# Kernel tuning notes

Hardware: AMD Instinct MI355X
Metric: run time of the kernel (lower is better)

## Reference

```python
import jax, jax.numpy as jnp
import numpy as np

B = 8192
G, K, D = 8, 1024, 64  # num_codebooks, codebook_size, code_dim
INIT_SCALE = 0.1


def setup_inputs() -> dict:
    key = jax.random.key(0)
    kz, kc = jax.random.split(key)
    z = jax.random.normal(kz, (B, G * D), dtype=jnp.float32)
    codebook = jax.random.uniform(kc, (G, K, D), dtype=jnp.float32,
                                  minval=-INIT_SCALE, maxval=INIT_SCALE)
    return {"z": z, "codebook": codebook}


def reference(z, codebook):
    # Eval-mode forward of GroupedVectorQuantizer (no EMA buffer mutation).
    b = z.shape[0]
    g, k, d = codebook.shape
    zg = z.reshape(b, g, d)                       # [B,G,D]
    # squared L2 distance via ||z||^2 + ||c||^2 - 2 z.c (avoids [B,G,K,D] diff tensor)
    z2 = jnp.sum(zg * zg, axis=-1, keepdims=True)           # [B,G,1]
    c2 = jnp.sum(codebook * codebook, axis=-1)[None]        # [1,G,K]
    zc = jnp.einsum('bgd,gkd->bgk', zg, codebook)           # [B,G,K]
    dist = z2 + c2 - 2.0 * zc                               # [B,G,K]
    indices = jnp.argmin(dist, axis=-1)                     # [B,G] int32
    # gather nearest codes per group
    zq = codebook[jnp.arange(g)[None, :], indices]          # [B,G,D]
    commitment_loss = jnp.mean((zg - jax.lax.stop_gradient(zq)) ** 2)
    codebook_loss = jnp.zeros((), dtype=z.dtype)
    # straight-through estimator
    z_st = zg + jax.lax.stop_gradient(zq - zg)
    quantized_flat = z_st.reshape(b, g * d)
    # codebook usage entropy / perplexity (pooled over batch and groups, as in torch)
    usage = jnp.zeros((k,), dtype=jnp.float32).at[indices.reshape(-1)].add(1.0) / (b * g)
    entropy = -jnp.sum(usage * jnp.log(usage + 1e-10))
    perplexity = jnp.exp(entropy)
    return quantized_flat, indices, commitment_loss, codebook_loss, entropy, perplexity
```

## Files before the change

### kernel.cpp

```cpp
#include <hip/hip_runtime.h>
#include <hip/hip_bf16.h>
#include <math.h>

#define NB 8192
#define NG 8
#define NK 1024
#define ND 64
#define GD 512
#define MARGIN 4.0e-4f
#define BIAS 16.0f

typedef __attribute__((ext_vector_type(8))) short short8;
typedef __attribute__((ext_vector_type(4))) float f32x4;

#define WS_C2_OFF   0
#define WS_C2B_OFF  32768
#define WS_STG_OFF  65536
#define WS_HIST_OFF (65536 + 2097152)
#define WS_PART_OFF (WS_HIST_OFF + 4096)

typedef const __attribute__((address_space(1))) unsigned int glds_src_t;
typedef __attribute__((address_space(3))) unsigned int glds_dst_t;

__device__ inline unsigned umin2(unsigned a, unsigned b) { return a < b ? a : b; }
__device__ inline unsigned umax2(unsigned a, unsigned b) { return a > b ? a : b; }

__device__ inline void bsplit(float v, short& hs, short& ls) {
    __hip_bfloat16 h = __float2bfloat16(v);
    float hf = __bfloat162float(h);
    __hip_bfloat16 l = __float2bfloat16(v - hf);
    hs = *reinterpret_cast<short*>(&h);
    ls = *reinterpret_cast<short*>(&l);
}

__device__ inline float wredsum(float v) {
#pragma unroll
    for (int st = 1; st < 64; st <<= 1) v += __shfl_xor(v, st);
    return v;
}

__global__ __launch_bounds__(64) void vq_prep(const float* __restrict__ cb,
                                              float* __restrict__ ws) {
    const int gid = blockIdx.x * 64 + threadIdx.x;
    const int g  = gid >> 10, k = gid & 1023;
    const int it = k >> 6,   row = k & 63;
    const float* c = cb + (size_t)gid * ND;
    char* base = (char*)ws + WS_STG_OFF + (size_t)(g * 16 + it) * 16384 + row * 128;

    float a0 = 0.f, a1 = 0.f, a2 = 0.f, a3 = 0.f;
#pragma unroll
    for (int j = 0; j < 8; ++j) {
        const float4 v0 = reinterpret_cast<const float4*>(c)[2 * j];
        const float4 v1 = reinterpret_cast<const float4*>(c)[2 * j + 1];
        a0 = fmaf(v0.x, v0.x, a0); a1 = fmaf(v0.y, v0.y, a1);
        a2 = fmaf(v0.z, v0.z, a2); a3 = fmaf(v0.w, v0.w, a3);
        a0 = fmaf(v1.x, v1.x, a0); a1 = fmaf(v1.y, v1.y, a1);
        a2 = fmaf(v1.z, v1.z, a2); a3 = fmaf(v1.w, v1.w, a3);
        short h0, l0, h1, l1, h2, l2, h3, l3;
        short h4, l4, h5, l5, h6, l6, h7, l7;
        bsplit(v0.x, h0, l0); bsplit(v0.y, h1, l1);
        bsplit(v0.z, h2, l2); bsplit(v0.w, h3, l3);
        bsplit(v1.x, h4, l4); bsplit(v1.y, h5, l5);
        bsplit(v1.z, h6, l6); bsplit(v1.w, h7, l7);
        short8 hs, ls;
        hs[0] = h0; hs[1] = h1; hs[2] = h2; hs[3] = h3;
        hs[4] = h4; hs[5] = h5; hs[6] = h6; hs[7] = h7;
        ls[0] = l0; ls[1] = l1; ls[2] = l2; ls[3] = l3;
        ls[4] = l4; ls[5] = l5; ls[6] = l6; ls[7] = l7;
        const int off = (j ^ (row & 7)) << 4;
        *reinterpret_cast<short8*>(base + off)        = hs;
        *reinterpret_cast<short8*>(base + 8192 + off) = ls;
    }
    const float c2s = (a0 + a1) + (a2 + a3);
    ((float*)((char*)ws + WS_C2_OFF))[gid]  = c2s;
    ((float*)((char*)ws + WS_C2B_OFF))[gid] = c2s + BIAS;
    if (gid < NK) ((unsigned*)((char*)ws + WS_HIST_OFF))[gid] = 0u;
}

__global__ __launch_bounds__(256, 4) void vq_score(const float* __restrict__ z,
                                                   const float* __restrict__ cb,
                                                   float* __restrict__ out,
                                                   float* __restrict__ ws) {
    __shared__ __align__(16) char smem[2][16384];
    __shared__ int winfo[4][16];
    const int tid  = threadIdx.x;
    const int w    = tid >> 6;
    const int lane = tid & 63;
    const int lo   = lane & 15, hi = lane >> 4;
    const int g    = blockIdx.y;
    const int rbase = blockIdx.x * 64 + w * 16;

    const char*  stg  = (const char*)ws + WS_STG_OFF + (size_t)g * 16 * 16384;
    const float* c2g  = (const float*)((const char*)ws + WS_C2_OFF) + g * NK;
    const float* c2bg = (const float*)((const char*)ws + WS_C2B_OFF) + g * NK;

    short8 Ah[2], Al[2];
#pragma unroll
    for (int ks = 0; ks < 2; ++ks) {
        const float* zp = z + (size_t)(rbase + lo) * GD + g * ND + ks * 32 + hi * 8;
        float vv[8];
        *reinterpret_cast<float4*>(&vv[0]) = reinterpret_cast<const float4*>(zp)[0];
        *reinterpret_cast<float4*>(&vv[4]) = reinterpret_cast<const float4*>(zp)[1];
#pragma unroll
        for (int e = 0; e < 8; ++e) {
            short hs, ls;
            bsplit(vv[e], hs, ls);
            Ah[ks][e] = hs;
            Al[ks][e] = ls;
        }
    }

    unsigned bestp[4][4], b2p[4][4];
#pragma unroll
    for (int n = 0; n < 4; ++n)
#pragma unroll
        for (int q = 0; q < 4; ++q) { bestp[n][q] = 0xFFFFFFFFu; b2p[n][q] = 0xFFFFFFFFu; }

    const int rowoff = lo * 128;
    const int swz0 = ((hi ^ (lo & 7)) << 4);
    const int swz1 = (((4 + hi) ^ (lo & 7)) << 4);
    char* lds0 = &smem[0][0];

    const char* src = stg;
    auto STAGE = [&](const char* s, unsigned dOff) {
#pragma unroll
        for (int i = 0; i < 4; ++i) {
            const int so = w * 4096 + i * 1024 + lane * 16;
            __builtin_amdgcn_global_load_lds(
                (glds_src_t*)(const void*)(s + so),
                (glds_dst_t*)(void*)(lds0 + dOff + so), 16, 0, 0);
        }
    };

    STAGE(src, 0u);
    src += 16384;
    __syncthreads();

#pragma unroll 1
    for (int it = 0; it < 16; ++it) {
        const int kb = it * 64;
        float c2v[4];
#pragma unroll
        for (int n = 0; n < 4; ++n) c2v[n] = c2bg[kb + n * 16 + lo];

        const unsigned cur = (unsigned)(it & 1) * 16384u;
        if (it < 15) { STAGE(src, cur ^ 16384u); src += 16384; }

        const char* bufc = lds0 + cur;
        f32x4 acc[4] = {{0.f,0.f,0.f,0.f},{0.f,0.f,0.f,0.f},{0.f,0.f,0.f,0.f},{0.f,0.f,0.f,0.f}};
#pragma unroll
        for (int ks = 0; ks < 2; ++ks) {
            short8 bh[4], bl[4];
#pragma unroll
            for (int n = 0; n < 4; ++n) {
                const int off = n * 2048 + rowoff + (ks ? swz1 : swz0);
                bh[n] = *reinterpret_cast<const short8*>(bufc + off);
                bl[n] = *reinterpret_cast<const short8*>(bufc + 8192 + off);
            }
#pragma unroll
            for (int n = 0; n < 4; ++n)
                acc[n] = __builtin_amdgcn_mfma_f32_16x16x32_bf16(
                    ks ? Ah[1] : Ah[0], bh[n], acc[n], 0, 0, 0);
#pragma unroll
            for (int n = 0; n < 4; ++n)
                acc[n] = __builtin_amdgcn_mfma_f32_16x16x32_bf16(
                    ks ? Ah[1] : Ah[0], bl[n], acc[n], 0, 0, 0);
#pragma unroll
            for (int n = 0; n < 4; ++n)
                acc[n] = __builtin_amdgcn_mfma_f32_16x16x32_bf16(
                    ks ? Al[1] : Al[0], bh[n], acc[n], 0, 0, 0);
        }

#pragma unroll
        for (int n = 0; n < 4; ++n)
#pragma unroll
            for (int q = 0; q < 4; ++q) {
                const float s = fmaf(-2.0f, acc[n][q], c2v[n]);
                const unsigned pk = (__float_as_uint(s) & 0xFFFFFFF0u) | (unsigned)it;
                b2p[n][q]   = umin2(b2p[n][q], umax2(bestp[n][q], pk));
                bestp[n][q] = umin2(bestp[n][q], pk);
            }
        __syncthreads();
    }

#pragma unroll
    for (int q = 0; q < 4; ++q) {
        unsigned pb = bestp[0][q], p2 = b2p[0][q];
        int nb = 0, n2 = 0;
#pragma unroll
        for (int n = 1; n < 4; ++n) {
            const unsigned cv  = bestp[n][q];
            const unsigned cb2 = b2p[n][q];
            const bool take = cv < pb;
            const unsigned loser  = take ? pb : cv;
            const int      nloser = take ? nb : n;
            pb = take ? cv : pb;
            nb = take ? n : nb;
            if (loser < p2 || (loser == p2 && nloser < n2)) { p2 = loser; n2 = nloser; }
            if (cb2 < p2 || (cb2 == p2 && n < n2))          { p2 = cb2;   n2 = n; }
        }
        int kq  = (int)(pb & 15u) * 64 + nb * 16 + lo;
        int kq2 = (int)(p2 & 15u) * 64 + n2 * 16 + lo;

#pragma unroll
        for (int st = 1; st < 16; st <<= 1) {
            const unsigned ob  = (unsigned)__shfl_xor((int)pb, st);
            const int      obk = __shfl_xor(kq, st);
            const unsigned ob2 = (unsigned)__shfl_xor((int)p2, st);
            const int      ok2 = __shfl_xor(kq2, st);
            const bool bet = (ob < pb) || (ob == pb && obk < kq);
            const unsigned lb  = bet ? pb : ob;
            const int      lk  = bet ? kq : obk;
            const unsigned wb2 = bet ? ob2 : p2;
            const int      wk2 = bet ? ok2 : kq2;
            const bool s2 = (lb < wb2) || (lb == wb2 && lk < wk2);
            p2  = s2 ? lb : wb2;
            kq2 = s2 ? lk : wk2;
            pb  = bet ? ob : pb;
            kq  = bet ? obk : kq;
        }
        if (lo == 0) {
            const float fpb = __uint_as_float(pb & 0xFFFFFFF0u);
            const float fp2 = __uint_as_float(p2 & 0xFFFFFFF0u);
            const int ridx = hi * 4 + q;
            const bool fl = (fp2 - fpb) <= MARGIN;
            winfo[w][ridx] = kq | (kq2 << 10) | (fl ? (1 << 20) : 0);
        }
    }
    asm volatile("s_waitcnt lgkmcnt(0)" ::: "memory");
    __builtin_amdgcn_sched_barrier(0);

    const float* cgrp = cb + (size_t)g * NK * ND;
    int* wif = &winfo[w][0];
    float esum = 0.f;
#pragma unroll 1
    for (int r = 0; r < 16; ++r) {
        const int info = wif[r];
        const int row  = rbase + r;
        const float zd = z[(size_t)row * GD + g * ND + lane];
        int win = info & 1023;

        if (info & (1 << 20)) {
            const int kalt = (info >> 10) & 1023;
            const float z2 = wredsum(zd * zd);
            const float c1 = cgrp[(size_t)win * ND + lane];
            const float d1 = (z2 + c2g[win]) - 2.0f * wredsum(zd * c1);
            const float c2 = cgrp[(size_t)kalt * ND + lane];
            const float d2 = (z2 + c2g[kalt]) - 2.0f * wredsum(zd * c2);
            if (d2 < d1 || (d2 == d1 && kalt < win)) win = kalt;
            if (lane == 0) wif[r] = win;
        }

        const float cw = cgrp[(size_t)win * ND + lane];
        out[(size_t)row * GD + g * ND + lane] = zd + (cw - zd);
        const float e = zd - cw;
        esum += e * e;
    }

    asm volatile("s_waitcnt lgkmcnt(0)" ::: "memory");
    __builtin_amdgcn_sched_barrier(0);
    if (lane < 16) {
        const int wv = wif[lane] & 1023;
        out[(size_t)NB * GD + (size_t)(rbase + lane) * NG + g] = (float)wv;
        atomicAdd((unsigned*)((char*)ws + WS_HIST_OFF) + wv, 1u);
    }

    esum = wredsum(esum);
    __shared__ float sh[4];
    if (lane == 0) sh[w] = esum;
    __syncthreads();
    if (tid == 0)
        ((float*)((char*)ws + WS_PART_OFF))[blockIdx.y * 128 + blockIdx.x] =
            (sh[0] + sh[1]) + (sh[2] + sh[3]);
}

__global__ __launch_bounds__(1024) void vq_final(const float* __restrict__ ws,
                                                 float* __restrict__ out) {
    const int t = threadIdx.x;
    __shared__ float se[1024];
    __shared__ float sc[1024];
    const unsigned cnt = ((const unsigned*)((const char*)ws + WS_HIST_OFF))[t];
    const float usage = (float)cnt * (1.0f / 65536.f);
    se[t] = -usage * logf(usage + 1e-10f);
    const float* part = (const float*)((const char*)ws + WS_PART_OFF);
    sc[t] = part[t];
    __syncthreads();
    for (int st = 512; st > 0; st >>= 1) {
        if (t < st) {
            se[t] += se[t + st];
            sc[t] += sc[t + st];
        }
        __syncthreads();
    }
    if (t == 0) {
        float* scal = out + (size_t)NB * GD + (size_t)NB * NG;
        scal[0] = sc[0] * (1.0f / ((float)NB * NG * ND));
        scal[1] = 0.0f;
        scal[2] = se[0];
        scal[3] = expf(se[0]);
    }
}

extern "C" void kernel_launch(void* const* d_in, const int* in_sizes, int n_in,
                              void* d_out, int out_size, void* d_ws, size_t ws_size,
                              hipStream_t stream) {
    const float* z  = (const float*)d_in[0];
    const float* cb = (const float*)d_in[1];
    float* out = (float*)d_out;
    float* ws  = (float*)d_ws;

    hipLaunchKernelGGL(vq_prep,  dim3(128),    dim3(64),   0, stream, cb, ws);
    hipLaunchKernelGGL(vq_score, dim3(128, 8), dim3(256),  0, stream, z, cb, out, ws);
    hipLaunchKernelGGL(vq_final, dim3(1),      dim3(1024), 0, stream, ws, out);
}
```

Measured before the change: 58.07 us.

## Give each wave a private double-buffered codebook stream and drop per-tile block barriers

The codebook staging layout changes from 64-row tiles to 16-row tiles. Each wave now streams its own 4KB tiles through a private LDS double buffer, paced by vmcnt waits instead of block-wide __syncthreads, and c2 is preloaded into LDS. Because each wave now scans all 1024 codes itself, the block fetches the staged codebook four times over, in exchange for removing the block barriers and lowering register pressure from 16 to 4 accumulators. The packed tile index grows to 6 bits, which costs mantissa precision, so the bias and the near-tie margin are retuned to keep ambiguous cases caught by the exact fallback.

```diff
diff --git a/kernel.cpp b/kernel.cpp
--- a/kernel.cpp
+++ b/kernel.cpp
@@ -7,8 +7,8 @@
 #define NK 1024
 #define ND 64
 #define GD 512
-#define MARGIN 4.0e-4f
-#define BIAS 16.0f
+#define MARGIN 6.0e-4f
+#define BIAS 8.0f
 
 typedef __attribute__((ext_vector_type(8))) short short8;
 typedef __attribute__((ext_vector_type(4))) float f32x4;
@@ -43,9 +43,9 @@
                                               float* __restrict__ ws) {
     const int gid = blockIdx.x * 64 + threadIdx.x;
     const int g  = gid >> 10, k = gid & 1023;
-    const int it = k >> 6,   row = k & 63;
+    const int t  = k >> 4,   row = k & 15;
     const float* c = cb + (size_t)gid * ND;
-    char* base = (char*)ws + WS_STG_OFF + (size_t)(g * 16 + it) * 16384 + row * 128;
+    char* base = (char*)ws + WS_STG_OFF + (size_t)(g * 64 + t) * 4096 + row * 128;
 
     float a0 = 0.f, a1 = 0.f, a2 = 0.f, a3 = 0.f;
 #pragma unroll
@@ -69,7 +69,7 @@
         ls[4] = l4; ls[5] = l5; ls[6] = l6; ls[7] = l7;
         const int off = (j ^ (row & 7)) << 4;
         *reinterpret_cast<short8*>(base + off)        = hs;
-        *reinterpret_cast<short8*>(base + 8192 + off) = ls;
+        *reinterpret_cast<short8*>(base + 2048 + off) = ls;
     }
     const float c2s = (a0 + a1) + (a2 + a3);
     ((float*)((char*)ws + WS_C2_OFF))[gid]  = c2s;
@@ -81,8 +81,10 @@
                                                    const float* __restrict__ cb,
                                                    float* __restrict__ out,
                                                    float* __restrict__ ws) {
-    __shared__ __align__(16) char smem[2][16384];
+    __shared__ __align__(16) char smem[4][8192];
+    __shared__ float c2sh[1024];
     __shared__ int winfo[4][16];
+    __shared__ float shred[4];
     const int tid  = threadIdx.x;
     const int w    = tid >> 6;
     const int lane = tid & 63;
@@ -90,7 +92,7 @@
     const int g    = blockIdx.y;
     const int rbase = blockIdx.x * 64 + w * 16;
 
-    const char*  stg  = (const char*)ws + WS_STG_OFF + (size_t)g * 16 * 16384;
+    const char*  stgg = (const char*)ws + WS_STG_OFF + (size_t)g * 64 * 4096;
     const float* c2g  = (const float*)((const char*)ws + WS_C2_OFF) + g * NK;
     const float* c2bg = (const float*)((const char*)ws + WS_C2B_OFF) + g * NK;
 
@@ -110,98 +112,76 @@
         }
     }
 
-    unsigned bestp[4][4], b2p[4][4];
-#pragma unroll
-    for (int n = 0; n < 4; ++n)
-#pragma unroll
-        for (int q = 0; q < 4; ++q) { bestp[n][q] = 0xFFFFFFFFu; b2p[n][q] = 0xFFFFFFFFu; }
+    char* mybuf = &smem[w][0];
+    auto STAGE = [&](const char* s, char* d) {
+#pragma unroll
+        for (int i = 0; i < 4; ++i)
+            __builtin_amdgcn_global_load_lds(
+                (glds_src_t*)(const void*)(s + i * 1024 + lane * 16),
+                (glds_dst_t*)(void*)(d + i * 1024 + lane * 16), 16, 0, 0);
+    };
+
+#pragma unroll
+    for (int i = 0; i < 4; ++i)
+        __builtin_amdgcn_global_load_lds(
+            (glds_src_t*)(const void*)(c2bg + w * 256 + i * 64 + lane),
+            (glds_dst_t*)(void*)(c2sh + w * 256 + i * 64 + lane), 4, 0, 0);
+    STAGE(stgg, mybuf);
+    STAGE(stgg + 4096, mybuf + 4096);
+    __syncthreads();
+
+    unsigned bestp[4], b2p[4];
+#pragma unroll
+    for (int q = 0; q < 4; ++q) { bestp[q] = 0xFFFFFFFFu; b2p[q] = 0xFFFFFFFFu; }
 
     const int rowoff = lo * 128;
     const int swz0 = ((hi ^ (lo & 7)) << 4);
     const int swz1 = (((4 + hi) ^ (lo & 7)) << 4);
-    char* lds0 = &smem[0][0];
-
-    const char* src = stg;
-    auto STAGE = [&](const char* s, unsigned dOff) {
-#pragma unroll
-        for (int i = 0; i < 4; ++i) {
-            const int so = w * 4096 + i * 1024 + lane * 16;
-            __builtin_amdgcn_global_load_lds(
-                (glds_src_t*)(const void*)(s + so),
-                (glds_dst_t*)(void*)(lds0 + dOff + so), 16, 0, 0);
-        }
+    const char* src = stgg + 8192;
+
+    auto TILE = [&](int t, const char* buf) {
+        const short8 bh0 = *reinterpret_cast<const short8*>(buf + rowoff + swz0);
+        const short8 bl0 = *reinterpret_cast<const short8*>(buf + 2048 + rowoff + swz0);
+        const short8 bh1 = *reinterpret_cast<const short8*>(buf + rowoff + swz1);
+        const short8 bl1 = *reinterpret_cast<const short8*>(buf + 2048 + rowoff + swz1);
+        asm volatile("s_waitcnt lgkmcnt(0)" ::: "memory");
+        __builtin_amdgcn_sched_barrier(0);
+        if (t < 62) {
+            STAGE(src, const_cast<char*>(buf));
+            src += 4096;
+        }
+        f32x4 acc = {0.f, 0.f, 0.f, 0.f};
+        acc = __builtin_amdgcn_mfma_f32_16x16x32_bf16(Ah[0], bh0, acc, 0, 0, 0);
+        acc = __builtin_amdgcn_mfma_f32_16x16x32_bf16(Ah[0], bl0, acc, 0, 0, 0);
+        acc = __builtin_amdgcn_mfma_f32_16x16x32_bf16(Al[0], bh0, acc, 0, 0, 0);
+        acc = __builtin_amdgcn_mfma_f32_16x16x32_bf16(Ah[1], bh1, acc, 0, 0, 0);
+        acc = __builtin_amdgcn_mfma_f32_16x16x32_bf16(Ah[1], bl1, acc, 0, 0, 0);
+        acc = __builtin_amdgcn_mfma_f32_16x16x32_bf16(Al[1], bh1, acc, 0, 0, 0);
+
+        const float c2v = c2sh[t * 16 + lo];
+#pragma unroll
+        for (int q = 0; q < 4; ++q) {
+            const float s = fmaf(-2.0f, acc[q], c2v);
+            const unsigned pk = (__float_as_uint(s) & 0xFFFFFFC0u) | (unsigned)t;
+            b2p[q]   = umin2(b2p[q], umax2(bestp[q], pk));
+            bestp[q] = umin2(bestp[q], pk);
+        }
+        if (t < 62)       asm volatile("s_waitcnt vmcnt(4)" ::: "memory");
+        else if (t == 62) asm volatile("s_waitcnt vmcnt(0)" ::: "memory");
+        __builtin_amdgcn_sched_barrier(0);
     };
 
-    STAGE(src, 0u);
-    src += 16384;
-    __syncthreads();
-
 #pragma unroll 1
-    for (int it = 0; it < 16; ++it) {
-        const int kb = it * 64;
-        float c2v[4];
-#pragma unroll
-        for (int n = 0; n < 4; ++n) c2v[n] = c2bg[kb + n * 16 + lo];
-
-        const unsigned cur = (unsigned)(it & 1) * 16384u;
-        if (it < 15) { STAGE(src, cur ^ 16384u); src += 16384; }
-
-        const char* bufc = lds0 + cur;
-        f32x4 acc[4] = {{0.f,0.f,0.f,0.f},{0.f,0.f,0.f,0.f},{0.f,0.f,0.f,0.f},{0.f,0.f,0.f,0.f}};
-#pragma unroll
-        for (int ks = 0; ks < 2; ++ks) {
-            short8 bh[4], bl[4];
-#pragma unroll
-            for (int n = 0; n < 4; ++n) {
-                const int off = n * 2048 + rowoff + (ks ? swz1 : swz0);
-                bh[n] = *reinterpret_cast<const short8*>(bufc + off);
-                bl[n] = *reinterpret_cast<const short8*>(bufc + 8192 + off);
-            }
-#pragma unroll
-            for (int n = 0; n < 4; ++n)
-                acc[n] = __builtin_amdgcn_mfma_f32_16x16x32_bf16(
-                    ks ? Ah[1] : Ah[0], bh[n], acc[n], 0, 0, 0);
-#pragma unroll
-            for (int n = 0; n < 4; ++n)
-                acc[n] = __builtin_amdgcn_mfma_f32_16x16x32_bf16(
-                    ks ? Ah[1] : Ah[0], bl[n], acc[n], 0, 0, 0);
-#pragma unroll
-            for (int n = 0; n < 4; ++n)
-                acc[n] = __builtin_amdgcn_mfma_f32_16x16x32_bf16(
-                    ks ? Al[1] : Al[0], bh[n], acc[n], 0, 0, 0);
-        }
-
-#pragma unroll
-        for (int n = 0; n < 4; ++n)
-#pragma unroll
-            for (int q = 0; q < 4; ++q) {
-                const float s = fmaf(-2.0f, acc[n][q], c2v[n]);
-                const unsigned pk = (__float_as_uint(s) & 0xFFFFFFF0u) | (unsigned)it;
-                b2p[n][q]   = umin2(b2p[n][q], umax2(bestp[n][q], pk));
-                bestp[n][q] = umin2(bestp[n][q], pk);
-            }
-        __syncthreads();
+    for (int t2 = 0; t2 < 32; ++t2) {
+        TILE(2 * t2,     mybuf);
+        TILE(2 * t2 + 1, mybuf + 4096);
     }
 
 #pragma unroll
     for (int q = 0; q < 4; ++q) {
-        unsigned pb = bestp[0][q], p2 = b2p[0][q];
-        int nb = 0, n2 = 0;
-#pragma unroll
-        for (int n = 1; n < 4; ++n) {
-            const unsigned cv  = bestp[n][q];
-            const unsigned cb2 = b2p[n][q];
-            const bool take = cv < pb;
-            const unsigned loser  = take ? pb : cv;
-            const int      nloser = take ? nb : n;
-            pb = take ? cv : pb;
-            nb = take ? n : nb;
-            if (loser < p2 || (loser == p2 && nloser < n2)) { p2 = loser; n2 = nloser; }
-            if (cb2 < p2 || (cb2 == p2 && n < n2))          { p2 = cb2;   n2 = n; }
-        }
-        int kq  = (int)(pb & 15u) * 64 + nb * 16 + lo;
-        int kq2 = (int)(p2 & 15u) * 64 + n2 * 16 + lo;
-
+        unsigned pb = bestp[q], p2 = b2p[q];
+        int kq  = (int)(pb & 63u) * 16 + lo;
+        int kq2 = (int)(p2 & 63u) * 16 + lo;
 #pragma unroll
         for (int st = 1; st < 16; st <<= 1) {
             const unsigned ob  = (unsigned)__shfl_xor((int)pb, st);
@@ -220,8 +200,8 @@
             kq  = bet ? obk : kq;
         }
         if (lo == 0) {
-            const float fpb = __uint_as_float(pb & 0xFFFFFFF0u);
-            const float fp2 = __uint_as_float(p2 & 0xFFFFFFF0u);
+            const float fpb = __uint_as_float(pb & 0xFFFFFFC0u);
+            const float fp2 = __uint_as_float(p2 & 0xFFFFFFC0u);
             const int ridx = hi * 4 + q;
             const bool fl = (fp2 - fpb) <= MARGIN;
             winfo[w][ridx] = kq | (kq2 << 10) | (fl ? (1 << 20) : 0);
@@ -266,12 +246,11 @@
     }
 
     esum = wredsum(esum);
-    __shared__ float sh[4];
-    if (lane == 0) sh[w] = esum;
+    if (lane == 0) shred[w] = esum;
     __syncthreads();
     if (tid == 0)
         ((float*)((char*)ws + WS_PART_OFF))[blockIdx.y * 128 + blockIdx.x] =
-            (sh[0] + sh[1]) + (sh[2] + sh[3]);
+            (shred[0] + shred[1]) + (shred[2] + shred[3]);
 }
 
 __global__ __launch_bounds__(1024) void vq_final(const float* __restrict__ ws,
```

New measurement: 67.76 us. 16.7% more time.
